# Kernel optimization log

Measured on AMD Instinct MI355X. Metric: run time of the kernel, lower is better.

Reference implementation:

```python
import jax, jax.numpy as jnp
import numpy as np

B, N, E, H = 2, 2048, 512, 8
D = E // H
SCALE_BASE = 512.0
EPS = 1e-6


def _xpos_tables(n, d):
    # XPOS (torchscale): per-dim scale ramp + standard sinusoidal freqs
    half = d // 2
    xscale = (np.arange(0, d, 2, dtype=np.float32) + 0.4 * d) / (1.4 * d)  # [half]
    min_pos = -(n // 2)
    power = (np.arange(min_pos, n + min_pos, dtype=np.float32) / SCALE_BASE)[:, None]
    scale = xscale[None, :] ** power                                       # [n, half]
    inv_freq = 1.0 / (10000.0 ** (np.arange(0, half, dtype=np.float32) / half))
    sinusoid = np.arange(n, dtype=np.float32)[:, None] * inv_freq[None, :]  # [n, half]
    return (jnp.asarray(np.sin(sinusoid), jnp.float32),
            jnp.asarray(np.cos(sinusoid), jnp.float32),
            jnp.asarray(scale, jnp.float32))


def _dup_interleave(m):
    # [n, half] -> [n, d], each column repeated twice interleaved
    return jnp.repeat(m, 2, axis=-1)


def _rotate_every_two(x):
    x1, x2 = x[..., ::2], x[..., 1::2]
    return jnp.stack((-x2, x1), axis=-1).reshape(x.shape)


def _apply_xpos(x, sin, cos, scale):
    s = _dup_interleave(sin * scale)  # [n, d]
    c = _dup_interleave(cos * scale)
    return x * c + _rotate_every_two(x) * s


def _decay_mask(n, dtype=jnp.float32):
    # gammas per head: 1 - exp(linspace(log(1/32), log(1/512), H))
    gammas = 1.0 - jnp.exp(jnp.linspace(np.log(1.0 / 32), np.log(1.0 / 512), H)).astype(dtype)
    pos = jnp.arange(n, dtype=dtype)
    dist = pos[:, None] - pos[None, :]                 # [n, s]
    dist_c = jnp.where(dist >= 0, dist, 0.0)
    return jnp.where(dist[None] >= 0, gammas[:, None, None] ** dist_c[None], 0.0)  # [h, n, s]


def _msr_forward(query, key, value, Wq, bq, Wk, bk, Wv, bv, Wg, bg, Wo, bo):
    b, n, e = query.shape
    q = (query @ Wq.T + bq).reshape(b, n, H, D).transpose(0, 2, 1, 3)  # [b,h,n,d]
    k = (key   @ Wk.T + bk).reshape(b, n, H, D).transpose(0, 2, 1, 3)
    v = (value @ Wv.T + bv).reshape(b, n, H, D).transpose(0, 2, 1, 3)

    sin, cos, scale = _xpos_tables(n, D)
    q = _apply_xpos(q, sin, cos, scale)
    k = _apply_xpos(k, sin, cos, 1.0 / scale)  # downscale=True

    k = k / jnp.asarray(np.sqrt(D), q.dtype)   # scale = head_dim ** 0.5
    mask = _decay_mask(n, q.dtype)             # [h,n,s]

    sim = jnp.einsum('bhnd,bhsd->bhns', q, k) * mask[None]
    ret = jnp.einsum('bhns,bhsd->bhnd', sim, v)  # [b,h,n,d]

    # GroupNorm(groups=H, channels=H, affine=False) on [(b n), h, d]:
    # normalize each (b, n, h) slice over its d elements
    mean = ret.mean(axis=-1, keepdims=True)
    var = ret.var(axis=-1, keepdims=True)
    ret = (ret - mean) / jnp.sqrt(var + EPS)

    ret = ret.transpose(0, 2, 1, 3).reshape(b, n, e)
    gate = jax.nn.silu(query @ Wg.T + bg)
    return (ret * gate) @ Wo.T + bo


def setup_inputs() -> dict:
    key = jax.random.key(0)
    ks = jax.random.split(key, 13)
    std = float(np.sqrt(2.0 / (E + E)))  # xavier_normal for square Linear
    mk = lambda k: jax.random.normal(k, (E, E), jnp.float32) * std
    return {
        'query': jax.random.normal(ks[0], (B, N, E), jnp.float32),
        'key':   jax.random.normal(ks[1], (B, N, E), jnp.float32),
        'value': jax.random.normal(ks[2], (B, N, E), jnp.float32),
        'Wq': mk(ks[3]), 'bq': jnp.zeros((E,), jnp.float32),
        'Wk': mk(ks[4]), 'bk': jnp.zeros((E,), jnp.float32),
        'Wv': mk(ks[5]), 'bv': jnp.zeros((E,), jnp.float32),
        'Wg': mk(ks[6]), 'bg': jnp.zeros((E,), jnp.float32),
        'Wo': mk(ks[7]), 'bo': jnp.zeros((E,), jnp.float32),
    }


def reference(query, key, value, Wq, bq, Wk, bk, Wv, bv, Wg, bg, Wo, bo):
    return _msr_forward(query, key, value, Wq, bq, Wk, bk, Wv, bv, Wg, bg, Wo, bo)
```

## Files before the change

### kernel.cpp

```cpp
#include <hip/hip_runtime.h>
#include <math.h>

#define Bc 2
#define Nc 2048
#define Ec 512
#define Hc 8
#define Dc 64
#define Mc 4096
#define NT 32
#define Cc 64

typedef short bf16x8 __attribute__((ext_vector_type(8)));
typedef float f32x4 __attribute__((ext_vector_type(4)));

#define GLOAD(g, l) __builtin_amdgcn_global_load_lds(                        \
    (const __attribute__((address_space(1))) unsigned*)(const void*)(g),     \
    (__attribute__((address_space(3))) unsigned*)(void*)(l), 16, 0, 0)

__device__ __forceinline__ unsigned short f2bf(float x) {
    union { float f; unsigned u; } v; v.f = x;
    unsigned r = v.u + 0x7fffu + ((v.u >> 16) & 1u);
    return (unsigned short)(r >> 16);
}
__device__ __forceinline__ float bf2f(unsigned short b) {
    union { float f; unsigned u; } v; v.u = ((unsigned)b) << 16;
    return v.f;
}

__device__ __forceinline__ float get_gamma(int h) {
    const float l0 = -3.4657359028f;
    const float l1 = -6.2383246250f;
    return 1.0f - expf(l0 + (l1 - l0) * ((float)h / 7.0f));
}

__global__ __launch_bounds__(256) void tables_kernel(float* __restrict__ sinS,
                                                     float* __restrict__ cosS,
                                                     float* __restrict__ sinIS,
                                                     float* __restrict__ cosIS) {
    int idx = blockIdx.x * 256 + threadIdx.x;
    if (idx >= Nc * 32) return;
    int n = idx >> 5;
    int i = idx & 31;
    float xscale = (2.0f * (float)i + 25.6f) / 89.6f;
    float power  = ((float)n - 1024.0f) / 512.0f;
    float scale  = powf(xscale, power);
    float inv_freq = powf(10000.0f, -(float)i / 32.0f);
    float ang = (float)n * inv_freq;
    float s = sinf(ang), c = cosf(ang);
    sinS[idx]  = s * scale;
    cosS[idx]  = c * scale;
    float rs = 1.0f / scale;
    sinIS[idx] = s * rs;
    cosIS[idx] = c * rs;
}

struct SplitArgs {
    const float* src[8];
    unsigned short* hi[8];
    unsigned short* lo[8];
    int n[8];
};

__global__ __launch_bounds__(256) void split_kernel(SplitArgs a) {
    int arr = blockIdx.y;
    int i4 = (blockIdx.x * 256 + threadIdx.x) * 4;
    if (i4 >= a.n[arr]) return;
    float4 v = *(const float4*)&a.src[arr][i4];
    ushort4 h, l;
    h.x = f2bf(v.x); l.x = f2bf(v.x - bf2f(h.x));
    h.y = f2bf(v.y); l.y = f2bf(v.y - bf2f(h.y));
    h.z = f2bf(v.z); l.z = f2bf(v.z - bf2f(h.z));
    h.w = f2bf(v.w); l.w = f2bf(v.w - bf2f(h.w));
    *(ushort4*)&a.hi[arr][i4] = h;
    *(ushort4*)&a.lo[arr][i4] = l;
}

template<int TM, int TN>
__global__ __launch_bounds__(256) void mgemm_kernel(
    const unsigned short* __restrict__ Xq_h, const unsigned short* __restrict__ Xq_l,
    const unsigned short* __restrict__ Xk_h, const unsigned short* __restrict__ Xk_l,
    const unsigned short* __restrict__ Xv_h, const unsigned short* __restrict__ Xv_l,
    const unsigned short* __restrict__ Xr_h, const unsigned short* __restrict__ Xr_l,
    const unsigned short* __restrict__ Wq_h, const unsigned short* __restrict__ Wq_l,
    const unsigned short* __restrict__ Wk_h, const unsigned short* __restrict__ Wk_l,
    const unsigned short* __restrict__ Wv_h, const unsigned short* __restrict__ Wv_l,
    const unsigned short* __restrict__ Wg_h, const unsigned short* __restrict__ Wg_l,
    const unsigned short* __restrict__ Wo_h, const unsigned short* __restrict__ Wo_l,
    const float* __restrict__ bq, const float* __restrict__ bk, const float* __restrict__ bv,
    const float* __restrict__ bg, const float* __restrict__ bo,
    float* __restrict__ Qr, float* __restrict__ Kr, float* __restrict__ Vr,
    float* __restrict__ G, float* __restrict__ Out,
    const float* __restrict__ sinS, const float* __restrict__ cosS,
    const float* __restrict__ sinIS, const float* __restrict__ cosIS,
    int mode_base)
{
    constexpr int MI = TM / 32;
    constexpr int NI = TN / 32;

    int mode = mode_base + blockIdx.z;
    const unsigned short *Xh, *Xl, *Wh, *Wl; const float* bias;
    switch (mode) {
        case 0:  Xh = Xq_h; Xl = Xq_l; Wh = Wq_h; Wl = Wq_l; bias = bq; break;
        case 1:  Xh = Xk_h; Xl = Xk_l; Wh = Wk_h; Wl = Wk_l; bias = bk; break;
        case 2:  Xh = Xv_h; Xl = Xv_l; Wh = Wv_h; Wl = Wv_l; bias = bv; break;
        case 3:  Xh = Xq_h; Xl = Xq_l; Wh = Wg_h; Wl = Wg_l; bias = bg; break;
        default: Xh = Xr_h; Xl = Xr_l; Wh = Wo_h; Wl = Wo_l; bias = bo; break;
    }

    __shared__ __align__(16) short lds[(TM + TN) * 64];
    constexpr int AL = TM * 32;
    constexpr int BH = TM * 64;
    constexpr int BL = TM * 64 + TN * 32;

    int tid  = threadIdx.x;
    int lane = tid & 63;
    int w    = tid >> 6;
    int wr   = w >> 1, wc = w & 1;
    int row0 = blockIdx.x * TM, col0 = blockIdx.y * TN;
    int lrow = lane & 15, lslot = lane >> 4;

    f32x4 acc[MI][NI];
    #pragma unroll
    for (int i = 0; i < MI; ++i)
        #pragma unroll
        for (int j = 0; j < NI; ++j) acc[i][j] = {0.f, 0.f, 0.f, 0.f};

    int aoff[MI], boff[NI];
    #pragma unroll
    for (int mi = 0; mi < MI; ++mi) {
        int r = wr * (TM / 2) + mi * 16 + lrow;
        aoff[mi] = (r * 4 + (lslot ^ ((r >> 1) & 3))) * 8;
    }
    #pragma unroll
    for (int ni = 0; ni < NI; ++ni) {
        int r = wc * (TN / 2) + ni * 16 + lrow;
        boff[ni] = (r * 4 + (lslot ^ ((r >> 1) & 3))) * 8;
    }

    for (int k0 = 0; k0 < Ec; k0 += 32) {
        #pragma unroll
        for (int i = 0; i < TM / 64; ++i) {
            int q = i * 256 + tid;
            int r = q >> 2;
            int sp = (q & 3) ^ ((r >> 1) & 3);
            int base = (i * 256 + (w << 6)) * 8;
            size_t ga = (size_t)(row0 + r) * Ec + k0 + sp * 8;
            GLOAD(Xh + ga, &lds[base]);
            GLOAD(Xl + ga, &lds[AL + base]);
        }
        #pragma unroll
        for (int i = 0; i < TN / 64; ++i) {
            int q = i * 256 + tid;
            int r = q >> 2;
            int sp = (q & 3) ^ ((r >> 1) & 3);
            int base = (i * 256 + (w << 6)) * 8;
            size_t gb = (size_t)(col0 + r) * Ec + k0 + sp * 8;
            GLOAD(Wh + gb, &lds[BH + base]);
            GLOAD(Wl + gb, &lds[BL + base]);
        }
        __syncthreads();

        bf16x8 ah[MI], al[MI], bh[NI], bl[NI];
        #pragma unroll
        for (int mi = 0; mi < MI; ++mi) {
            ah[mi] = *(const bf16x8*)&lds[aoff[mi]];
            al[mi] = *(const bf16x8*)&lds[AL + aoff[mi]];
        }
        #pragma unroll
        for (int ni = 0; ni < NI; ++ni) {
            bh[ni] = *(const bf16x8*)&lds[BH + boff[ni]];
            bl[ni] = *(const bf16x8*)&lds[BL + boff[ni]];
        }
        #pragma unroll
        for (int mi = 0; mi < MI; ++mi)
            #pragma unroll
            for (int ni = 0; ni < NI; ++ni) {
                acc[mi][ni] = __builtin_amdgcn_mfma_f32_16x16x32_bf16(ah[mi], bh[ni], acc[mi][ni], 0, 0, 0);
                acc[mi][ni] = __builtin_amdgcn_mfma_f32_16x16x32_bf16(ah[mi], bl[ni], acc[mi][ni], 0, 0, 0);
                acc[mi][ni] = __builtin_amdgcn_mfma_f32_16x16x32_bf16(al[mi], bh[ni], acc[mi][ni], 0, 0, 0);
            }
        __syncthreads();
    }

    int quad = lane >> 4;
    #pragma unroll
    for (int mi = 0; mi < MI; ++mi) {
        #pragma unroll
        for (int reg = 0; reg < 4; ++reg) {
            int R  = row0 + wr * (TM / 2) + mi * 16 + quad * 4 + reg;
            int bb = R >> 11;
            int n  = R & 2047;
            #pragma unroll
            for (int ni = 0; ni < NI; ++ni) {
                int c = col0 + wc * (TN / 2) + ni * 16 + lrow;
                float x = acc[mi][ni][reg] + bias[c];
                if (mode <= 1) {
                    float p = __shfl_xor(x, 1, 64);
                    int h = c >> 6, d = c & 63, pr = d >> 1;
                    const float* st = (mode == 0) ? sinS : sinIS;
                    const float* ct = (mode == 0) ? cosS : cosIS;
                    float sv = st[n * 32 + pr], cv = ct[n * 32 + pr];
                    float y = (c & 1) ? fmaf(x, cv,  p * sv)
                                      : fmaf(x, cv, -p * sv);
                    if (mode == 1) y *= 0.125f;
                    float* dst = (mode == 0) ? Qr : Kr;
                    dst[(((size_t)(bb * Hc + h)) * Nc + n) * Dc + d] = y;
                } else if (mode == 2) {
                    int h = c >> 6, d = c & 63;
                    Vr[(((size_t)(bb * Hc + h)) * Nc + n) * Dc + d] = x;
                } else if (mode == 3) {
                    G[(size_t)R * Ec + c] = x / (1.0f + expf(-x));
                } else {
                    Out[(size_t)R * Ec + c] = x;
                }
            }
        }
    }
}

__global__ __launch_bounds__(256) void phaseA_kernel(const float* __restrict__ Kr,
                                                     const float* __restrict__ Vr,
                                                     float* __restrict__ L)
{
    int bh = blockIdx.x;
    int t  = blockIdx.y;
    float gamma = get_gamma(bh & 7);
    float lg = logf(gamma);

    __shared__ float Ks[64][68];
    __shared__ float Vs[64][68];

    int tid = threadIdx.x;
    const float* Kc = Kr + (size_t)(bh * Nc + t * Cc) * Dc;
    const float* Vc = Vr + (size_t)(bh * Nc + t * Cc) * Dc;

    #pragma unroll
    for (int i = 0; i < 4; ++i) {
        int f = tid + i * 256;
        int s = f >> 4;
        int d = (f & 15) << 2;
        float w = expf(lg * (float)(Cc - s));
        float4 kv = *(const float4*)&Kc[s * Dc + d];
        float4 ks = {kv.x * w, kv.y * w, kv.z * w, kv.w * w};
        *(float4*)&Ks[s][d] = ks;
        float4 vv = *(const float4*)&Vc[s * Dc + d];
        *(float4*)&Vs[s][d] = vv;
    }
    __syncthreads();

    int tx = tid & 15, ty = tid >> 4;
    float acc[4][4];
    #pragma unroll
    for (int i = 0; i < 4; ++i)
        #pragma unroll
        for (int j = 0; j < 4; ++j) acc[i][j] = 0.0f;

    for (int s = 0; s < 64; ++s) {
        float4 a = *(const float4*)&Ks[s][ty * 4];
        float4 b = *(const float4*)&Vs[s][tx * 4];
        float av[4] = {a.x, a.y, a.z, a.w};
        float bv[4] = {b.x, b.y, b.z, b.w};
        #pragma unroll
        for (int i = 0; i < 4; ++i)
            #pragma unroll
            for (int j = 0; j < 4; ++j)
                acc[i][j] = fmaf(av[i], bv[j], acc[i][j]);
    }

    float* Lp = L + (size_t)(bh * NT + t) * 4096;
    #pragma unroll
    for (int i = 0; i < 4; ++i) {
        float4 o = {acc[i][0], acc[i][1], acc[i][2], acc[i][3]};
        *(float4*)&Lp[(ty * 4 + i) * 64 + tx * 4] = o;
    }
}

__global__ __launch_bounds__(256) void scan_kernel(const float* __restrict__ L,
                                                   float* __restrict__ Sst)
{
    int bh = blockIdx.x;
    int part = blockIdx.y;
    int tid = threadIdx.x;
    float gamma = get_gamma(bh & 7);
    float g64 = expf(logf(gamma) * 64.0f);

    float4 s = {0.0f, 0.0f, 0.0f, 0.0f};
    size_t base = (size_t)bh * NT * 4096 + part * 1024 + tid * 4;
    const float* Lp = L + base;
    float* Sp = Sst + base;
    for (int t = 0; t < NT; ++t) {
        *(float4*)&Sp[(size_t)t * 4096] = s;
        float4 l = *(const float4*)&Lp[(size_t)t * 4096];
        s.x = s.x * g64 + l.x;
        s.y = s.y * g64 + l.y;
        s.z = s.z * g64 + l.z;
        s.w = s.w * g64 + l.w;
    }
}

__global__ __launch_bounds__(256) void phaseC_kernel(
    const float* __restrict__ Qr, const float* __restrict__ Kr, const float* __restrict__ Vr,
    const float* __restrict__ Sst, const float* __restrict__ G,
    unsigned short* __restrict__ retGh, unsigned short* __restrict__ retGl)
{
    int bh = blockIdx.x, t = blockIdx.y;
    int b = bh >> 3, h = bh & 7;
    float gamma = get_gamma(h);
    float lg = logf(gamma);

    __shared__ float QsT[64][68];
    __shared__ float KsT[64][68];
    __shared__ float Ss[64][68];

    int tid = threadIdx.x;
    const float* Qc = Qr + (size_t)(bh * Nc + t * Cc) * Dc;
    const float* Kc = Kr + (size_t)(bh * Nc + t * Cc) * Dc;
    const float* Sp = Sst + (size_t)(bh * NT + t) * 4096;

    #pragma unroll
    for (int i = 0; i < 4; ++i) {
        int f = tid + i * 256;
        int r = f >> 4;
        int d = (f & 15) << 2;
        float wq = expf(lg * (float)r);
        float4 q = *(const float4*)&Qc[r * Dc + d];
        QsT[d + 0][r] = q.x * wq; QsT[d + 1][r] = q.y * wq;
        QsT[d + 2][r] = q.z * wq; QsT[d + 3][r] = q.w * wq;
        float wk = expf(-lg * (float)r);
        float4 kk = *(const float4*)&Kc[r * Dc + d];
        KsT[d + 0][r] = kk.x * wk; KsT[d + 1][r] = kk.y * wk;
        KsT[d + 2][r] = kk.z * wk; KsT[d + 3][r] = kk.w * wk;
        float4 sv = *(const float4*)&Sp[r * 64 + d];
        *(float4*)&Ss[r][d] = sv;
    }
    __syncthreads();

    int tx = tid & 15, ty = tid >> 4;
    float accA[4][4], accO[4][4];
    #pragma unroll
    for (int i = 0; i < 4; ++i)
        #pragma unroll
        for (int j = 0; j < 4; ++j) { accA[i][j] = 0.0f; accO[i][j] = 0.0f; }

    for (int d = 0; d < 64; ++d) {
        float4 a  = *(const float4*)&QsT[d][ty * 4];
        float4 kb = *(const float4*)&KsT[d][tx * 4];
        float4 sb = *(const float4*)&Ss[d][tx * 4];
        float av[4] = {a.x, a.y, a.z, a.w};
        float kv[4] = {kb.x, kb.y, kb.z, kb.w};
        float sv[4] = {sb.x, sb.y, sb.z, sb.w};
        #pragma unroll
        for (int i = 0; i < 4; ++i)
            #pragma unroll
            for (int j = 0; j < 4; ++j) {
                accA[i][j] = fmaf(av[i], kv[j], accA[i][j]);
                accO[i][j] = fmaf(av[i], sv[j], accO[i][j]);
            }
    }
    __syncthreads();

    #pragma unroll
    for (int i = 0; i < 4; ++i) {
        int gi = ty * 4 + i;
        #pragma unroll
        for (int j = 0; j < 4; ++j) {
            int gj = tx * 4 + j;
            KsT[gj][gi] = (gj <= gi) ? accA[i][j] : 0.0f;
        }
    }
    const float* Vc = Vr + (size_t)(bh * Nc + t * Cc) * Dc;
    #pragma unroll
    for (int i = 0; i < 4; ++i) {
        int f = tid + i * 256;
        int r = f >> 4;
        int d = (f & 15) << 2;
        float4 vv = *(const float4*)&Vc[r * Dc + d];
        *(float4*)&QsT[r][d] = vv;
    }
    __syncthreads();

    for (int j = 0; j < 64; ++j) {
        float4 a = *(const float4*)&KsT[j][ty * 4];
        float4 v = *(const float4*)&QsT[j][tx * 4];
        float av[4] = {a.x, a.y, a.z, a.w};
        float vv[4] = {v.x, v.y, v.z, v.w};
        #pragma unroll
        for (int i = 0; i < 4; ++i)
            #pragma unroll
            for (int jj = 0; jj < 4; ++jj)
                accO[i][jj] = fmaf(av[i], vv[jj], accO[i][jj]);
    }

    #pragma unroll
    for (int i = 0; i < 4; ++i) {
        float sum = accO[i][0] + accO[i][1] + accO[i][2] + accO[i][3];
        float sq  = accO[i][0] * accO[i][0] + accO[i][1] * accO[i][1]
                  + accO[i][2] * accO[i][2] + accO[i][3] * accO[i][3];
        #pragma unroll
        for (int m = 1; m < 16; m <<= 1) {
            sum += __shfl_xor(sum, m, 64);
            sq  += __shfl_xor(sq,  m, 64);
        }
        float mean = sum * (1.0f / 64.0f);
        float var  = sq * (1.0f / 64.0f) - mean * mean;
        float rinv = rsqrtf(var + 1e-6f);
        #pragma unroll
        for (int jj = 0; jj < 4; ++jj)
            accO[i][jj] = (accO[i][jj] - mean) * rinv;
    }

    #pragma unroll
    for (int i = 0; i < 4; ++i) {
        int n = t * Cc + ty * 4 + i;
        size_t idx = ((size_t)b * Nc + n) * Ec + h * Dc + tx * 4;
        float4 g = *(const float4*)&G[idx];
        float o0 = accO[i][0] * g.x, o1 = accO[i][1] * g.y;
        float o2 = accO[i][2] * g.z, o3 = accO[i][3] * g.w;
        ushort4 hh, ll;
        hh.x = f2bf(o0); ll.x = f2bf(o0 - bf2f(hh.x));
        hh.y = f2bf(o1); ll.y = f2bf(o1 - bf2f(hh.y));
        hh.z = f2bf(o2); ll.z = f2bf(o2 - bf2f(hh.z));
        hh.w = f2bf(o3); ll.w = f2bf(o3 - bf2f(hh.w));
        *(ushort4*)&retGh[idx] = hh;
        *(ushort4*)&retGl[idx] = ll;
    }
}

extern "C" void kernel_launch(void* const* d_in, const int* in_sizes, int n_in,
                              void* d_out, int out_size, void* d_ws, size_t ws_size,
                              hipStream_t stream) {
    const float* query = (const float*)d_in[0];
    const float* key   = (const float*)d_in[1];
    const float* value = (const float*)d_in[2];
    const float* Wq = (const float*)d_in[3];
    const float* bq = (const float*)d_in[4];
    const float* Wk = (const float*)d_in[5];
    const float* bk = (const float*)d_in[6];
    const float* Wv = (const float*)d_in[7];
    const float* bv = (const float*)d_in[8];
    const float* Wg = (const float*)d_in[9];
    const float* bg = (const float*)d_in[10];
    const float* Wo = (const float*)d_in[11];
    const float* bo = (const float*)d_in[12];
    float* out = (float*)d_out;

    float* wsf = (float*)d_ws;
    const size_t SZ = (size_t)Bc * Nc * Ec;

    float* Qr = wsf;
    float* Kr = Qr + SZ;
    float* Vr = Kr + SZ;
    float* G  = Vr + SZ;

    unsigned short* Xq_h = (unsigned short*)(wsf + 4 * SZ);
    unsigned short* Xq_l = Xq_h + SZ;
    unsigned short* Xk_h = Xq_l + SZ;
    unsigned short* Xk_l = Xk_h + SZ;
    unsigned short* Xv_h = Xk_l + SZ;
    unsigned short* Xv_l = Xv_h + SZ;
    float* L   = wsf + 4 * SZ;
    float* Sst = wsf + 5 * SZ;
    unsigned short* retGh = (unsigned short*)(wsf + 6 * SZ);
    unsigned short* retGl = retGh + SZ;

    const size_t WSZ = (size_t)Ec * Ec;
    unsigned short* Wp = (unsigned short*)(wsf + 7 * SZ);
    unsigned short* Wq_h = Wp;            unsigned short* Wq_l = Wp + WSZ;
    unsigned short* Wk_h = Wp + 2 * WSZ;  unsigned short* Wk_l = Wp + 3 * WSZ;
    unsigned short* Wv_h = Wp + 4 * WSZ;  unsigned short* Wv_l = Wp + 5 * WSZ;
    unsigned short* Wg_h = Wp + 6 * WSZ;  unsigned short* Wg_l = Wp + 7 * WSZ;
    unsigned short* Wo_h = Wp + 8 * WSZ;  unsigned short* Wo_l = Wp + 9 * WSZ;

    float* tab = wsf + 7 * SZ + (10 * WSZ) / 2;
    float* sinS  = tab;
    float* cosS  = sinS + Nc * 32;
    float* sinIS = cosS + Nc * 32;
    float* cosIS = sinIS + Nc * 32;

    tables_kernel<<<dim3((Nc * 32 + 255) / 256), dim3(256), 0, stream>>>(sinS, cosS, sinIS, cosIS);

    SplitArgs sa;
    sa.src[0] = query; sa.hi[0] = Xq_h; sa.lo[0] = Xq_l; sa.n[0] = (int)SZ;
    sa.src[1] = key;   sa.hi[1] = Xk_h; sa.lo[1] = Xk_l; sa.n[1] = (int)SZ;
    sa.src[2] = value; sa.hi[2] = Xv_h; sa.lo[2] = Xv_l; sa.n[2] = (int)SZ;
    sa.src[3] = Wq;    sa.hi[3] = Wq_h; sa.lo[3] = Wq_l; sa.n[3] = (int)WSZ;
    sa.src[4] = Wk;    sa.hi[4] = Wk_h; sa.lo[4] = Wk_l; sa.n[4] = (int)WSZ;
    sa.src[5] = Wv;    sa.hi[5] = Wv_h; sa.lo[5] = Wv_l; sa.n[5] = (int)WSZ;
    sa.src[6] = Wg;    sa.hi[6] = Wg_h; sa.lo[6] = Wg_l; sa.n[6] = (int)WSZ;
    sa.src[7] = Wo;    sa.hi[7] = Wo_h; sa.lo[7] = Wo_l; sa.n[7] = (int)WSZ;
    split_kernel<<<dim3(2048, 8), dim3(256), 0, stream>>>(sa);

    mgemm_kernel<128, 64><<<dim3(Mc / 128, Ec / 64, 4), dim3(256), 0, stream>>>(
        Xq_h, Xq_l, Xk_h, Xk_l, Xv_h, Xv_l, retGh, retGl,
        Wq_h, Wq_l, Wk_h, Wk_l, Wv_h, Wv_l, Wg_h, Wg_l, Wo_h, Wo_l,
        bq, bk, bv, bg, bo, Qr, Kr, Vr, G, out,
        sinS, cosS, sinIS, cosIS, 0);

    phaseA_kernel<<<dim3(Bc * Hc, NT), dim3(256), 0, stream>>>(Kr, Vr, L);
    scan_kernel<<<dim3(Bc * Hc, 4), dim3(256), 0, stream>>>(L, Sst);
    phaseC_kernel<<<dim3(Bc * Hc, NT), dim3(256), 0, stream>>>(Qr, Kr, Vr, Sst, G, retGh, retGl);

    mgemm_kernel<64, 64><<<dim3(Mc / 64, Ec / 64, 1), dim3(256), 0, stream>>>(
        Xq_h, Xq_l, Xk_h, Xk_l, Xv_h, Xv_l, retGh, retGl,
        Wq_h, Wq_l, Wk_h, Wk_l, Wv_h, Wv_l, Wg_h, Wg_l, Wo_h, Wo_l,
        bq, bk, bv, bg, bo, Qr, Kr, Vr, G, out,
        sinS, cosS, sinIS, cosIS, 4);
}
```

Baseline: 185.7 us.

## Double-buffer GEMM LDS loads, merge table and split kernels, widen tile

The split-bf16 GEMM now double-buffers its LDS tiles. It issues the next k-slice's global-to-LDS loads before computing on the current one and uses explicit vmcnt waits and raw barriers instead of __syncthreads. The sin/cos table kernel is folded into the split kernel as an extra grid row, which removes one launch. The projection GEMM tile grows from 128x64 to 128x128. This aims to hide load latency and launch overhead, at the cost of twice the LDS, fewer blocks and hand-tuned waitcnt counts that must match the number of loads issued.

```diff
diff --git a/kernel.cpp b/kernel.cpp
--- a/kernel.cpp
+++ b/kernel.cpp
@@ -33,27 +33,6 @@
     return 1.0f - expf(l0 + (l1 - l0) * ((float)h / 7.0f));
 }
 
-__global__ __launch_bounds__(256) void tables_kernel(float* __restrict__ sinS,
-                                                     float* __restrict__ cosS,
-                                                     float* __restrict__ sinIS,
-                                                     float* __restrict__ cosIS) {
-    int idx = blockIdx.x * 256 + threadIdx.x;
-    if (idx >= Nc * 32) return;
-    int n = idx >> 5;
-    int i = idx & 31;
-    float xscale = (2.0f * (float)i + 25.6f) / 89.6f;
-    float power  = ((float)n - 1024.0f) / 512.0f;
-    float scale  = powf(xscale, power);
-    float inv_freq = powf(10000.0f, -(float)i / 32.0f);
-    float ang = (float)n * inv_freq;
-    float s = sinf(ang), c = cosf(ang);
-    sinS[idx]  = s * scale;
-    cosS[idx]  = c * scale;
-    float rs = 1.0f / scale;
-    sinIS[idx] = s * rs;
-    cosIS[idx] = c * rs;
-}
-
 struct SplitArgs {
     const float* src[8];
     unsigned short* hi[8];
@@ -61,18 +40,40 @@
     int n[8];
 };
 
-__global__ __launch_bounds__(256) void split_kernel(SplitArgs a) {
-    int arr = blockIdx.y;
+__global__ __launch_bounds__(256) void prep_kernel(SplitArgs a,
+                                                   float* __restrict__ sinS,
+                                                   float* __restrict__ cosS,
+                                                   float* __restrict__ sinIS,
+                                                   float* __restrict__ cosIS) {
+    int y = blockIdx.y;
+    if (y == 8) {
+        int idx = blockIdx.x * 256 + threadIdx.x;
+        if (idx >= Nc * 32) return;
+        int n = idx >> 5;
+        int i = idx & 31;
+        float xscale = (2.0f * (float)i + 25.6f) / 89.6f;
+        float power  = ((float)n - 1024.0f) / 512.0f;
+        float scale  = powf(xscale, power);
+        float inv_freq = powf(10000.0f, -(float)i / 32.0f);
+        float ang = (float)n * inv_freq;
+        float s = sinf(ang), c = cosf(ang);
+        sinS[idx]  = s * scale;
+        cosS[idx]  = c * scale;
+        float rs = 1.0f / scale;
+        sinIS[idx] = s * rs;
+        cosIS[idx] = c * rs;
+        return;
+    }
     int i4 = (blockIdx.x * 256 + threadIdx.x) * 4;
-    if (i4 >= a.n[arr]) return;
-    float4 v = *(const float4*)&a.src[arr][i4];
+    if (i4 >= a.n[y]) return;
+    float4 v = *(const float4*)&a.src[y][i4];
     ushort4 h, l;
     h.x = f2bf(v.x); l.x = f2bf(v.x - bf2f(h.x));
     h.y = f2bf(v.y); l.y = f2bf(v.y - bf2f(h.y));
     h.z = f2bf(v.z); l.z = f2bf(v.z - bf2f(h.z));
     h.w = f2bf(v.w); l.w = f2bf(v.w - bf2f(h.w));
-    *(ushort4*)&a.hi[arr][i4] = h;
-    *(ushort4*)&a.lo[arr][i4] = l;
+    *(ushort4*)&a.hi[y][i4] = h;
+    *(ushort4*)&a.lo[y][i4] = l;
 }
 
 template<int TM, int TN>
@@ -94,8 +95,13 @@
     const float* __restrict__ sinIS, const float* __restrict__ cosIS,
     int mode_base)
 {
-    constexpr int MI = TM / 32;
-    constexpr int NI = TN / 32;
+    constexpr int MI  = TM / 32;
+    constexpr int NI  = TN / 32;
+    constexpr int BUF = (TM + TN) * 64;
+    constexpr int GL  = (TM / 64 + TN / 64) * 2;
+    constexpr int AL  = TM * 32;
+    constexpr int BHo = TM * 64;
+    constexpr int BLo = TM * 64 + TN * 32;
 
     int mode = mode_base + blockIdx.z;
     const unsigned short *Xh, *Xl, *Wh, *Wl; const float* bias;
@@ -107,10 +113,7 @@
         default: Xh = Xr_h; Xl = Xr_l; Wh = Wo_h; Wl = Wo_l; bias = bo; break;
     }
 
-    __shared__ __align__(16) short lds[(TM + TN) * 64];
-    constexpr int AL = TM * 32;
-    constexpr int BH = TM * 64;
-    constexpr int BL = TM * 64 + TN * 32;
+    __shared__ __align__(16) short lds[2 * BUF];
 
     int tid  = threadIdx.x;
     int lane = tid & 63;
@@ -137,7 +140,8 @@
         boff[ni] = (r * 4 + (lslot ^ ((r >> 1) & 3))) * 8;
     }
 
-    for (int k0 = 0; k0 < Ec; k0 += 32) {
+    auto stage = [&](int buf, int k0) {
+        short* l = &lds[buf * BUF];
         #pragma unroll
         for (int i = 0; i < TM / 64; ++i) {
             int q = i * 256 + tid;
@@ -145,8 +149,8 @@
             int sp = (q & 3) ^ ((r >> 1) & 3);
             int base = (i * 256 + (w << 6)) * 8;
             size_t ga = (size_t)(row0 + r) * Ec + k0 + sp * 8;
-            GLOAD(Xh + ga, &lds[base]);
-            GLOAD(Xl + ga, &lds[AL + base]);
+            GLOAD(Xh + ga, &l[base]);
+            GLOAD(Xl + ga, &l[AL + base]);
         }
         #pragma unroll
         for (int i = 0; i < TN / 64; ++i) {
@@ -155,31 +159,47 @@
             int sp = (q & 3) ^ ((r >> 1) & 3);
             int base = (i * 256 + (w << 6)) * 8;
             size_t gb = (size_t)(col0 + r) * Ec + k0 + sp * 8;
-            GLOAD(Wh + gb, &lds[BH + base]);
-            GLOAD(Wl + gb, &lds[BL + base]);
-        }
-        __syncthreads();
-
-        bf16x8 ah[MI], al[MI], bh[NI], bl[NI];
+            GLOAD(Wh + gb, &l[BHo + base]);
+            GLOAD(Wl + gb, &l[BLo + base]);
+        }
+    };
+
+    stage(0, 0);
+    for (int t = 0; t < Ec / 32; ++t) {
+        int cur = t & 1;
+        if (t < Ec / 32 - 1) {
+            stage(cur ^ 1, (t + 1) * 32);
+            if constexpr (GL == 8) asm volatile("s_waitcnt vmcnt(8)" ::: "memory");
+            else                   asm volatile("s_waitcnt vmcnt(4)" ::: "memory");
+        } else {
+            asm volatile("s_waitcnt vmcnt(0)" ::: "memory");
+        }
+        __builtin_amdgcn_s_barrier();
+        __builtin_amdgcn_sched_barrier(0);
+
+        const short* l = &lds[cur * BUF];
+        bf16x8 ah[MI], al2[MI], bh[NI], bl[NI];
         #pragma unroll
         for (int mi = 0; mi < MI; ++mi) {
-            ah[mi] = *(const bf16x8*)&lds[aoff[mi]];
-            al[mi] = *(const bf16x8*)&lds[AL + aoff[mi]];
+            ah[mi]  = *(const bf16x8*)&l[aoff[mi]];
+            al2[mi] = *(const bf16x8*)&l[AL + aoff[mi]];
         }
         #pragma unroll
         for (int ni = 0; ni < NI; ++ni) {
-            bh[ni] = *(const bf16x8*)&lds[BH + boff[ni]];
-            bl[ni] = *(const bf16x8*)&lds[BL + boff[ni]];
+            bh[ni] = *(const bf16x8*)&l[BHo + boff[ni]];
+            bl[ni] = *(const bf16x8*)&l[BLo + boff[ni]];
         }
         #pragma unroll
         for (int mi = 0; mi < MI; ++mi)
             #pragma unroll
             for (int ni = 0; ni < NI; ++ni) {
-                acc[mi][ni] = __builtin_amdgcn_mfma_f32_16x16x32_bf16(ah[mi], bh[ni], acc[mi][ni], 0, 0, 0);
-                acc[mi][ni] = __builtin_amdgcn_mfma_f32_16x16x32_bf16(ah[mi], bl[ni], acc[mi][ni], 0, 0, 0);
-                acc[mi][ni] = __builtin_amdgcn_mfma_f32_16x16x32_bf16(al[mi], bh[ni], acc[mi][ni], 0, 0, 0);
+                acc[mi][ni] = __builtin_amdgcn_mfma_f32_16x16x32_bf16(ah[mi],  bh[ni], acc[mi][ni], 0, 0, 0);
+                acc[mi][ni] = __builtin_amdgcn_mfma_f32_16x16x32_bf16(ah[mi],  bl[ni], acc[mi][ni], 0, 0, 0);
+                acc[mi][ni] = __builtin_amdgcn_mfma_f32_16x16x32_bf16(al2[mi], bh[ni], acc[mi][ni], 0, 0, 0);
             }
-        __syncthreads();
+        asm volatile("s_waitcnt lgkmcnt(0)" ::: "memory");
+        __builtin_amdgcn_sched_barrier(0);
+        __builtin_amdgcn_s_barrier();
     }
 
     int quad = lane >> 4;
@@ -477,8 +497,6 @@
     float* sinIS = cosS + Nc * 32;
     float* cosIS = sinIS + Nc * 32;
 
-    tables_kernel<<<dim3((Nc * 32 + 255) / 256), dim3(256), 0, stream>>>(sinS, cosS, sinIS, cosIS);
-
     SplitArgs sa;
     sa.src[0] = query; sa.hi[0] = Xq_h; sa.lo[0] = Xq_l; sa.n[0] = (int)SZ;
     sa.src[1] = key;   sa.hi[1] = Xk_h; sa.lo[1] = Xk_l; sa.n[1] = (int)SZ;
@@ -488,9 +506,9 @@
     sa.src[5] = Wv;    sa.hi[5] = Wv_h; sa.lo[5] = Wv_l; sa.n[5] = (int)WSZ;
     sa.src[6] = Wg;    sa.hi[6] = Wg_h; sa.lo[6] = Wg_l; sa.n[6] = (int)WSZ;
     sa.src[7] = Wo;    sa.hi[7] = Wo_h; sa.lo[7] = Wo_l; sa.n[7] = (int)WSZ;
-    split_kernel<<<dim3(2048, 8), dim3(256), 0, stream>>>(sa);
-
-    mgemm_kernel<128, 64><<<dim3(Mc / 128, Ec / 64, 4), dim3(256), 0, stream>>>(
+    prep_kernel<<<dim3(2048, 9), dim3(256), 0, stream>>>(sa, sinS, cosS, sinIS, cosIS);
+
+    mgemm_kernel<128, 128><<<dim3(Mc / 128, Ec / 128, 4), dim3(256), 0, stream>>>(
         Xq_h, Xq_l, Xk_h, Xk_l, Xv_h, Xv_l, retGh, retGl,
         Wq_h, Wq_l, Wk_h, Wk_l, Wv_h, Wv_l, Wg_h, Wg_l, Wo_h, Wo_l,
         bq, bk, bv, bg, bo, Qr, Kr, Vr, G, out,
```

Result: no change. 186.9 us (+0.7%).
